# Kernel tuning notes

Measured on AMD Instinct MI355X. Metric: run time of the kernel, lower is better.

Reference implementation:

```python
import jax, jax.numpy as jnp
import numpy as np

N, IN, D, H, C, G = 50000, 128, 64, 4, 10, 64
E_RAND = 800000
NEG_SLOPE = 0.2  # DGL GATConv default LeakyReLU slope


def setup_inputs() -> dict:
    key = jax.random.key(0)
    ks = jax.random.split(key, 20)
    h = jax.random.normal(ks[0], (N, IN), jnp.float32)
    # random edges + self-loops so every dst has at least one in-edge
    src = jnp.concatenate([jax.random.randint(ks[1], (E_RAND,), 0, N), jnp.arange(N)]).astype(jnp.int32)
    dst = jnp.concatenate([jax.random.randint(ks[2], (E_RAND,), 0, N), jnp.arange(N)]).astype(jnp.int32)
    graph_id = jnp.sort(jax.random.randint(ks[3], (N,), 0, G)).astype(jnp.int32)
    w = lambda k, s: jax.random.normal(k, s, jnp.float32) * 0.1
    return {
        "h": h, "src": src, "dst": dst, "graph_id": graph_id,
        "W0": w(ks[4], (IN, H * D)),    "al0": w(ks[5], (H, D)), "ar0": w(ks[6], (H, D)),
        "W1": w(ks[7], (H * D, H * D)), "al1": w(ks[8], (H, D)), "ar1": w(ks[9], (H, D)),
        "W2": w(ks[10], (H * D, H * D)), "al2": w(ks[11], (H, D)), "ar2": w(ks[12], (H, D)),
        "W3": w(ks[13], (H * D, D)),    "al3": w(ks[14], (1, D)), "ar3": w(ks[15], (1, D)),
        "fc1_w": w(ks[16], (D, D)), "fc1_b": jnp.zeros((D,), jnp.float32),
        "fc2_w": w(ks[17], (D, C)), "fc2_b": jnp.zeros((C,), jnp.float32),
    }


def gat_layer(x, W, al, ar, src, dst):
    """DGL GATConv: z=xW; e=LeakyReLU(a_l.z_src + a_r.z_dst); softmax over in-edges of dst; out=sum alpha*z_src."""
    nh, nd = al.shape
    z = (x @ W).reshape(N, nh, nd)                      # [N,H,D]
    el = jnp.sum(z * al, axis=-1)                       # [N,H]
    er = jnp.sum(z * ar, axis=-1)                       # [N,H]
    e = jax.nn.leaky_relu(el[src] + er[dst], NEG_SLOPE)  # [E,H]
    m = jax.ops.segment_max(e, dst, num_segments=N)     # per-dst max (stable softmax)
    ex = jnp.exp(e - m[dst])
    den = jax.ops.segment_sum(ex, dst, num_segments=N)
    alpha = ex / den[dst]                               # [E,H]
    msg = alpha[:, :, None] * z[src]                    # [E,H,D]
    return jax.ops.segment_sum(msg, dst, num_segments=N)  # [N,H,D]


def reference(h, src, dst, graph_id, W0, al0, ar0, W1, al1, ar1, W2, al2, ar2,
              W3, al3, ar3, fc1_w, fc1_b, fc2_w, fc2_b):
    x = jax.nn.relu(gat_layer(h, W0, al0, ar0, src, dst).reshape(N, -1))
    x = jax.nn.relu(gat_layer(x, W1, al1, ar1, src, dst).reshape(N, -1))
    x = jax.nn.relu(gat_layer(x, W2, al2, ar2, src, dst).reshape(N, -1))
    x = jax.nn.relu(gat_layer(x, W3, al3, ar3, src, dst).reshape(N, -1))  # [N,D] (1 head)
    # AvgPooling: mean node features per graph
    counts = jax.ops.segment_sum(jnp.ones((N,), x.dtype), graph_id, num_segments=G)
    pooled = jax.ops.segment_sum(x, graph_id, num_segments=G) / jnp.maximum(counts, 1.0)[:, None]
    y = jax.nn.elu(pooled @ fc1_w + fc1_b)
    y = y @ fc2_w + fc2_b
    return jax.nn.log_softmax(y, axis=0)  # original applies log_softmax over dim=0
```

## Files before the change

### kernel.cpp

```cpp
#include <hip/hip_runtime.h>
#include <hip/hip_bf16.h>
#include <math.h>

#define NN 50000
#define IN_F 128
#define DD 64
#define HH 4
#define CC 10
#define GG 64
#define NEG_SLOPE 0.2f

typedef __attribute__((ext_vector_type(8))) short bf16x8;
typedef __attribute__((ext_vector_type(4))) float f32x4;
typedef __attribute__((ext_vector_type(4))) unsigned short u16x4;

__device__ inline ushort f2bf(float f) {
    unsigned u = __float_as_uint(f);
    unsigned r = (u + 0x7fffu + ((u >> 16) & 1u)) >> 16;
    return (ushort)r;
}
__device__ inline float bf2f(ushort b) { return __uint_as_float(((unsigned)b) << 16); }

__device__ inline float wave_max(float v) {
#pragma unroll
    for (int o = 32; o > 0; o >>= 1) v = fmaxf(v, __shfl_xor(v, o));
    return v;
}
__device__ inline float wave_sum(float v) {
#pragma unroll
    for (int o = 32; o > 0; o >>= 1) v += __shfl_xor(v, o);
    return v;
}

__global__ void hist_kernel(const int* __restrict__ dst, int E, int* __restrict__ counts) {
    int i = blockIdx.x * blockDim.x + threadIdx.x;
    if (i < E) atomicAdd(&counts[dst[i]], 1);
}

__global__ __launch_bounds__(256) void scan_blk(const int* __restrict__ counts,
                                                int* __restrict__ excl,
                                                int* __restrict__ bsum, int n) {
    __shared__ int sh[256];
    int t = threadIdx.x;
    int i = blockIdx.x * 256 + t;
    int v = (i < n) ? counts[i] : 0;
    sh[t] = v;
    __syncthreads();
#pragma unroll
    for (int o = 1; o < 256; o <<= 1) {
        int u = (t >= o) ? sh[t - o] : 0;
        __syncthreads();
        sh[t] += u;
        __syncthreads();
    }
    if (i < n) excl[i] = sh[t] - v;
    if (t == 255) bsum[blockIdx.x] = sh[255];
}

__global__ __launch_bounds__(256) void scan_top(int* __restrict__ bsum, int nb) {
    __shared__ int sh[256];
    int t = threadIdx.x;
    int v = (t < nb) ? bsum[t] : 0;
    sh[t] = v;
    __syncthreads();
#pragma unroll
    for (int o = 1; o < 256; o <<= 1) {
        int u = (t >= o) ? sh[t - o] : 0;
        __syncthreads();
        sh[t] += u;
        __syncthreads();
    }
    if (t < nb) bsum[t] = sh[t] - v;
}

__global__ __launch_bounds__(256) void scan_fin(const int* __restrict__ excl,
                                                const int* __restrict__ bsum,
                                                int* __restrict__ row_ptr,
                                                int* __restrict__ fill, int n, int E) {
    int i = blockIdx.x * blockDim.x + threadIdx.x;
    if (i < n) {
        int r = excl[i] + bsum[i >> 8];
        row_ptr[i] = r;
        fill[i] = r;
    }
    if (i == 0) row_ptr[n] = E;
}

__global__ void scatter_kernel(const int* __restrict__ src, const int* __restrict__ dst,
                               int E, int* __restrict__ fill, int* __restrict__ col_src) {
    int i = blockIdx.x * blockDim.x + threadIdx.x;
    if (i < E) {
        int p = atomicAdd(&fill[dst[i]], 1);
        col_src[p] = src[i];
    }
}

__global__ void wconv_kernel(const float* __restrict__ W, int K, int N,
                             ushort* __restrict__ thi) {
    int i = blockIdx.x * blockDim.x + threadIdx.x;
    if (i >= K * N) return;
    int k = i / N, n = i - k * N;
    size_t o = ((size_t)(k >> 5) * N + n) * 32 + (k & 31);
    thi[o] = f2bf(W[i]);
}

template <int N, int H, bool AF32>
__global__ __launch_bounds__(256) void gemm_mfma_eler(
    const void* __restrict__ A0,
    const ushort* __restrict__ Wthi,
    ushort* __restrict__ zt, const float* __restrict__ al, const float* __restrict__ ar,
    float* __restrict__ el, float* __restrict__ er, int M, int K) {
    constexpr int NT = N / 16;
    __shared__ ushort Bh[2][N][34];
    const int t = threadIdx.x;
    const int w = t >> 6, lane = t & 63;
    const int cl = lane & 15, g = lane >> 4;
    const int bm = blockIdx.x * 64;
    const int arow = bm + 16 * w + cl;
    const bool aval = arow < M;
    const size_t abase = (size_t)arow * K;
    const float* Af = (const float*)A0;
    const ushort* Abf = (const ushort*)A0;

    f32x4 acc[NT];
#pragma unroll
    for (int nt = 0; nt < NT; ++nt) acc[nt] = (f32x4){0.f, 0.f, 0.f, 0.f};

    const int nkb = K >> 5;

    float4 fa0 = {0, 0, 0, 0}, fa1 = {0, 0, 0, 0};
    bf16x8 araw = {0, 0, 0, 0, 0, 0, 0, 0};
    if (aval) {
        if (AF32) {
            fa0 = *(const float4*)(Af + abase + g * 8);
            fa1 = *(const float4*)(Af + abase + g * 8 + 4);
        } else {
            araw = *(const bf16x8*)(Abf + abase + g * 8);
        }
    }
    if (t < N) {
        const float4* gs = (const float4*)(Wthi + (size_t)t * 32);
#pragma unroll
        for (int q = 0; q < 4; ++q) *(float4*)&Bh[0][t][q * 8] = gs[q];
    }
    __syncthreads();

    for (int kb = 0; kb < nkb; ++kb) {
        const int cur = kb & 1;
        bf16x8 a_cur;
        if (AF32) {
            float fv[8] = {fa0.x, fa0.y, fa0.z, fa0.w, fa1.x, fa1.y, fa1.z, fa1.w};
#pragma unroll
            for (int q = 0; q < 8; ++q) a_cur[q] = (short)f2bf(fv[q]);
        } else {
            a_cur = araw;
        }
        float4 rn0, rn1, rn2, rn3;
        const bool pf = (kb + 1 < nkb);
        if (pf && t < N) {
            const float4* gs = (const float4*)(Wthi + ((size_t)(kb + 1) * N + t) * 32);
            rn0 = gs[0]; rn1 = gs[1]; rn2 = gs[2]; rn3 = gs[3];
        }
        if (pf && aval) {
            if (AF32) {
                fa0 = *(const float4*)(Af + abase + (kb + 1) * 32 + g * 8);
                fa1 = *(const float4*)(Af + abase + (kb + 1) * 32 + g * 8 + 4);
            } else {
                araw = *(const bf16x8*)(Abf + abase + (kb + 1) * 32 + g * 8);
            }
        }
#pragma unroll
        for (int nt = 0; nt < NT; ++nt) {
            bf16x8 b_hi = *(const bf16x8*)&Bh[cur][16 * nt + cl][g * 8];
            acc[nt] = __builtin_amdgcn_mfma_f32_16x16x32_bf16(a_cur, b_hi, acc[nt], 0, 0, 0);
        }
        if (pf && t < N) {
            *(float4*)&Bh[cur ^ 1][t][0]  = rn0;
            *(float4*)&Bh[cur ^ 1][t][8]  = rn1;
            *(float4*)&Bh[cur ^ 1][t][16] = rn2;
            *(float4*)&Bh[cur ^ 1][t][24] = rn3;
        }
        __syncthreads();
    }

    const int r0 = bm + 16 * w + 4 * g;
    if (H == 4) {
#pragma unroll
        for (int tt = 0; tt < 4; ++tt) {
#pragma unroll
            for (int j = 0; j < 4; ++j) {
                int r = r0 + j;
                if (r < M) {
                    u16x4 pv;
#pragma unroll
                    for (int h = 0; h < 4; ++h) pv[h] = f2bf(acc[4 * h + tt][j]);
                    *(u16x4*)&zt[(size_t)r * 256 + (16 * tt + cl) * 4] = pv;
                }
            }
        }
    } else {
#pragma unroll
        for (int nt = 0; nt < NT; ++nt) {
#pragma unroll
            for (int j = 0; j < 4; ++j) {
                int r = r0 + j;
                if (r < M) zt[(size_t)r * N + 16 * nt + cl] = f2bf(acc[nt][j]);
            }
        }
    }
#pragma unroll
    for (int h = 0; h < H; ++h) {
        float pl[4] = {0.f, 0.f, 0.f, 0.f};
        float pr[4] = {0.f, 0.f, 0.f, 0.f};
#pragma unroll
        for (int tt = 0; tt < 4; ++tt) {
            int nt = 4 * h + tt;
            float av = al[h * DD + 16 * tt + cl];
            float rv = ar[h * DD + 16 * tt + cl];
#pragma unroll
            for (int j = 0; j < 4; ++j) {
                pl[j] += acc[nt][j] * av;
                pr[j] += acc[nt][j] * rv;
            }
        }
#pragma unroll
        for (int j = 0; j < 4; ++j) {
#pragma unroll
            for (int o = 1; o < 16; o <<= 1) {
                pl[j] += __shfl_xor(pl[j], o);
                pr[j] += __shfl_xor(pr[j], o);
            }
        }
        if (cl == 0) {
#pragma unroll
            for (int j = 0; j < 4; ++j) {
                int r = r0 + j;
                if (r < M) {
                    el[(size_t)r * H + h] = pl[j];
                    er[(size_t)r * H + h] = pr[j];
                }
            }
        }
    }
}

template <int H, bool OUTBF>
__global__ __launch_bounds__(256) void agg_fused(const ushort* __restrict__ zt,
                                                 const float* __restrict__ el,
                                                 const float* __restrict__ er,
                                                 const int* __restrict__ row_ptr,
                                                 const int* __restrict__ col_src,
                                                 float* __restrict__ outf,
                                                 ushort* __restrict__ obf) {
    __shared__ float alf[4][64][H];
    __shared__ int als[4][64];
    const int wid = threadIdx.x >> 6;
    const int lane = threadIdx.x & 63;
    int v = blockIdx.x * 4 + wid;
    if (v >= NN) return;
    int start = row_ptr[v], end = row_ptr[v + 1];
    int deg = end - start;
    float erd[H], acc[H];
#pragma unroll
    for (int h = 0; h < H; ++h) {
        erd[h] = er[(size_t)v * H + h];
        acc[h] = 0.f;
    }

    auto agg_chunk = [&](int cnt) {
        int j = 0;
        for (; j + 4 <= cnt; j += 4) {
            int s0 = als[wid][j + 0], s1 = als[wid][j + 1];
            int s2 = als[wid][j + 2], s3 = als[wid][j + 3];
            if (H == 4) {
                f32x4 a0 = *(const f32x4*)&alf[wid][j + 0][0];
                f32x4 a1 = *(const f32x4*)&alf[wid][j + 1][0];
                f32x4 a2 = *(const f32x4*)&alf[wid][j + 2][0];
                f32x4 a3 = *(const f32x4*)&alf[wid][j + 3][0];
                u16x4 z0 = *(const u16x4*)&zt[(size_t)s0 * 256 + lane * 4];
                u16x4 z1 = *(const u16x4*)&zt[(size_t)s1 * 256 + lane * 4];
                u16x4 z2 = *(const u16x4*)&zt[(size_t)s2 * 256 + lane * 4];
                u16x4 z3 = *(const u16x4*)&zt[(size_t)s3 * 256 + lane * 4];
#pragma unroll
                for (int h = 0; h < 4; ++h) {
                    acc[h] += a0[h] * bf2f(z0[h]);
                    acc[h] += a1[h] * bf2f(z1[h]);
                    acc[h] += a2[h] * bf2f(z2[h]);
                    acc[h] += a3[h] * bf2f(z3[h]);
                }
            } else {
                float a0 = alf[wid][j + 0][0], a1 = alf[wid][j + 1][0];
                float a2 = alf[wid][j + 2][0], a3 = alf[wid][j + 3][0];
                ushort z0 = zt[(size_t)s0 * 64 + lane];
                ushort z1 = zt[(size_t)s1 * 64 + lane];
                ushort z2 = zt[(size_t)s2 * 64 + lane];
                ushort z3 = zt[(size_t)s3 * 64 + lane];
                acc[0] += a0 * bf2f(z0);
                acc[0] += a1 * bf2f(z1);
                acc[0] += a2 * bf2f(z2);
                acc[0] += a3 * bf2f(z3);
            }
        }
        for (; j < cnt; ++j) {
            int s = als[wid][j];
            if (H == 4) {
                f32x4 a = *(const f32x4*)&alf[wid][j][0];
                u16x4 z = *(const u16x4*)&zt[(size_t)s * 256 + lane * 4];
#pragma unroll
                for (int h = 0; h < 4; ++h) acc[h] += a[h] * bf2f(z[h]);
            } else {
                acc[0] += alf[wid][j][0] * bf2f(zt[(size_t)s * 64 + lane]);
            }
        }
    };

    if (deg <= 64) {
        bool valid = lane < deg;
        int s = col_src[valid ? start + lane : start];
        als[wid][lane] = s;
        float e[H];
        if (H == 4) {
            f32x4 ev = *(const f32x4*)&el[(size_t)s * 4];
#pragma unroll
            for (int h = 0; h < 4; ++h) {
                float x = ev[h] + erd[h];
                x = (x >= 0.f) ? x : NEG_SLOPE * x;
                e[h] = valid ? x : -1e30f;
            }
        } else {
            float x = el[s] + erd[0];
            x = (x >= 0.f) ? x : NEG_SLOPE * x;
            e[0] = valid ? x : -1e30f;
        }
#pragma unroll
        for (int h = 0; h < H; ++h) {
            float m = wave_max(e[h]);
            float ex = valid ? __expf(e[h] - m) : 0.f;
            float den = wave_sum(ex);
            alf[wid][lane][h] = ex * (1.f / den);
        }
        __builtin_amdgcn_wave_barrier();
        agg_chunk(deg);
    } else {
        float m[H];
#pragma unroll
        for (int h = 0; h < H; ++h) m[h] = -1e30f;
        for (int base = start; base < end; base += 64) {
            int i = base + lane;
            bool valid = i < end;
            int s = col_src[valid ? i : start];
#pragma unroll
            for (int h = 0; h < H; ++h) {
                float x = el[(size_t)s * H + h] + erd[h];
                x = (x >= 0.f) ? x : NEG_SLOPE * x;
                m[h] = fmaxf(m[h], valid ? x : -1e30f);
            }
        }
        float den[H];
#pragma unroll
        for (int h = 0; h < H; ++h) {
            m[h] = wave_max(m[h]);
            den[h] = 0.f;
        }
        for (int base = start; base < end; base += 64) {
            int i = base + lane;
            bool valid = i < end;
            int s = col_src[valid ? i : start];
#pragma unroll
            for (int h = 0; h < H; ++h) {
                float x = el[(size_t)s * H + h] + erd[h];
                x = (x >= 0.f) ? x : NEG_SLOPE * x;
                den[h] += valid ? __expf(x - m[h]) : 0.f;
            }
        }
        float inv[H];
#pragma unroll
        for (int h = 0; h < H; ++h) inv[h] = 1.f / wave_sum(den[h]);
        for (int base = start; base < end; base += 64) {
            int i = base + lane;
            bool valid = i < end;
            int s = col_src[valid ? i : start];
            als[wid][lane] = s;
#pragma unroll
            for (int h = 0; h < H; ++h) {
                float x = el[(size_t)s * H + h] + erd[h];
                x = (x >= 0.f) ? x : NEG_SLOPE * x;
                alf[wid][lane][h] = valid ? __expf(x - m[h]) * inv[h] : 0.f;
            }
            __builtin_amdgcn_wave_barrier();
            int cnt = min(64, end - base);
            agg_chunk(cnt);
            __builtin_amdgcn_wave_barrier();
        }
    }

#pragma unroll
    for (int h = 0; h < H; ++h) {
        float r = acc[h];
        r = (r > 0.f) ? r : 0.f;
        size_t idx = (size_t)v * H * DD + h * DD + lane;
        if (OUTBF) {
            obf[idx] = f2bf(r);
        } else {
            outf[idx] = r;
        }
    }
}

__device__ inline int lower_bound_dev(const int* a, int n, int v) {
    int lo = 0, hi = n;
    while (lo < hi) {
        int mid = (lo + hi) >> 1;
        if (a[mid] < v) lo = mid + 1; else hi = mid;
    }
    return lo;
}

__global__ __launch_bounds__(256) void pool_kernel(const float* __restrict__ x,
                                                   const int* __restrict__ gid,
                                                   float* __restrict__ pooled,
                                                   float* __restrict__ gcnt) {
    int g = blockIdx.x;
    int start = lower_bound_dev(gid, NN, g);
    int end = lower_bound_dev(gid, NN, g + 1);
    int lane = threadIdx.x & 63;
    int w = threadIdx.x >> 6;
    float acc = 0.f;
    for (int i = start + w; i < end; i += 4) acc += x[(size_t)i * DD + lane];
    __shared__ float red[4][DD];
    red[w][lane] = acc;
    __syncthreads();
    if (w == 0) {
        float s = red[0][lane] + red[1][lane] + red[2][lane] + red[3][lane];
        pooled[g * DD + lane] = s;
        if (lane == 0) gcnt[g] = (float)(end - start);
    }
}

__global__ __launch_bounds__(64) void head_kernel(const float* __restrict__ pooled,
                                                  const float* __restrict__ gcnt,
                                                  const float* __restrict__ fc1w,
                                                  const float* __restrict__ fc1b,
                                                  const float* __restrict__ fc2w,
                                                  const float* __restrict__ fc2b,
                                                  float* __restrict__ out) {
    __shared__ float P[GG][DD + 1];
    __shared__ float Y1[GG][DD + 1];
    int g = threadIdx.x;
    float c = fmaxf(gcnt[g], 1.0f);
    for (int k = 0; k < DD; ++k) P[g][k] = pooled[g * DD + k] / c;
    __syncthreads();
    for (int j = 0; j < DD; ++j) {
        float s = fc1b[j];
        for (int k = 0; k < DD; ++k) s += P[g][k] * fc1w[k * DD + j];
        Y1[g][j] = (s > 0.f) ? s : expm1f(s);
    }
    __syncthreads();
    float y2[CC];
    for (int c2 = 0; c2 < CC; ++c2) {
        float s = fc2b[c2];
        for (int j = 0; j < DD; ++j) s += Y1[g][j] * fc2w[j * CC + c2];
        y2[c2] = s;
    }
    for (int c2 = 0; c2 < CC; ++c2) {
        float m = y2[c2];
#pragma unroll
        for (int o = 32; o > 0; o >>= 1) m = fmaxf(m, __shfl_xor(m, o));
        float sexp = __expf(y2[c2] - m);
#pragma unroll
        for (int o = 32; o > 0; o >>= 1) sexp += __shfl_xor(sexp, o);
        out[g * CC + c2] = y2[c2] - m - logf(sexp);
    }
}

extern "C" void kernel_launch(void* const* d_in, const int* in_sizes, int n_in,
                              void* d_out, int out_size, void* d_ws, size_t ws_size,
                              hipStream_t stream) {
    const float* h    = (const float*)d_in[0];
    const int* src    = (const int*)d_in[1];
    const int* dst    = (const int*)d_in[2];
    const int* gid    = (const int*)d_in[3];
    const float* W0   = (const float*)d_in[4];
    const float* al0  = (const float*)d_in[5];
    const float* ar0  = (const float*)d_in[6];
    const float* W1   = (const float*)d_in[7];
    const float* al1  = (const float*)d_in[8];
    const float* ar1  = (const float*)d_in[9];
    const float* W2   = (const float*)d_in[10];
    const float* al2  = (const float*)d_in[11];
    const float* ar2  = (const float*)d_in[12];
    const float* W3   = (const float*)d_in[13];
    const float* al3  = (const float*)d_in[14];
    const float* ar3  = (const float*)d_in[15];
    const float* fc1w = (const float*)d_in[16];
    const float* fc1b = (const float*)d_in[17];
    const float* fc2w = (const float*)d_in[18];
    const float* fc2b = (const float*)d_in[19];
    const int E = in_sizes[1];

    char* wsb = (char*)d_ws;
    size_t off = 0;
    auto alloc = [&](size_t bytes) -> void* {
        void* p = wsb + off;
        off = (off + bytes + 255) & ~(size_t)255;
        return p;
    };
    ushort* zt      = (ushort*)alloc((size_t)NN * 256 * 2);
    ushort* Abf     = (ushort*)alloc((size_t)NN * 256 * 2);
    float*  bufA    = (float*)alloc((size_t)NN * DD * 4);
    float*  el      = (float*)alloc((size_t)NN * HH * 4);
    float*  er      = (float*)alloc((size_t)NN * HH * 4);
    int*    counts  = (int*)alloc((size_t)NN * 4);
    int*    row_ptr = (int*)alloc((size_t)(NN + 1) * 4);
    int*    fill    = (int*)alloc((size_t)NN * 4);
    int*    excl    = (int*)alloc((size_t)NN * 4);
    int*    bsum    = (int*)alloc((size_t)256 * 4);
    int*    col_src = (int*)alloc((size_t)E * 4);
    float*  pooled  = (float*)alloc((size_t)GG * DD * 4);
    float*  gcnt    = (float*)alloc((size_t)GG * 4);
    ushort* w0h     = (ushort*)alloc((size_t)IN_F * 256 * 2);
    ushort* w1h     = (ushort*)alloc((size_t)256 * 256 * 2);
    ushort* w2h     = (ushort*)alloc((size_t)256 * 256 * 2);
    ushort* w3h     = (ushort*)alloc((size_t)256 * 64 * 2);

    hipMemsetAsync(counts, 0, (size_t)NN * 4, stream);
    int eg = (E + 255) / 256;
    const int nScanBlk = (NN + 255) / 256;
    hist_kernel<<<eg, 256, 0, stream>>>(dst, E, counts);
    scan_blk<<<nScanBlk, 256, 0, stream>>>(counts, excl, bsum, NN);
    scan_top<<<1, 256, 0, stream>>>(bsum, nScanBlk);
    scan_fin<<<nScanBlk, 256, 0, stream>>>(excl, bsum, row_ptr, fill, NN, E);
    scatter_kernel<<<eg, 256, 0, stream>>>(src, dst, E, fill, col_src);

    wconv_kernel<<<(IN_F * 256 + 255) / 256, 256, 0, stream>>>(W0, IN_F, 256, w0h);
    wconv_kernel<<<(256 * 256 + 255) / 256, 256, 0, stream>>>(W1, 256, 256, w1h);
    wconv_kernel<<<(256 * 256 + 255) / 256, 256, 0, stream>>>(W2, 256, 256, w2h);
    wconv_kernel<<<(256 * 64 + 255) / 256, 256, 0, stream>>>(W3, 256, 64, w3h);

    const int gemmGrid = (NN + 63) / 64;
    const int waveBlocks = (NN + 3) / 4;

    gemm_mfma_eler<256, 4, true><<<gemmGrid, 256, 0, stream>>>(h, w0h, zt, al0, ar0, el, er, NN, IN_F);
    agg_fused<4, true><<<waveBlocks, 256, 0, stream>>>(zt, el, er, row_ptr, col_src, nullptr, Abf);

    gemm_mfma_eler<256, 4, false><<<gemmGrid, 256, 0, stream>>>(Abf, w1h, zt, al1, ar1, el, er, NN, 256);
    agg_fused<4, true><<<waveBlocks, 256, 0, stream>>>(zt, el, er, row_ptr, col_src, nullptr, Abf);

    gemm_mfma_eler<256, 4, false><<<gemmGrid, 256, 0, stream>>>(Abf, w2h, zt, al2, ar2, el, er, NN, 256);
    agg_fused<4, true><<<waveBlocks, 256, 0, stream>>>(zt, el, er, row_ptr, col_src, nullptr, Abf);

    gemm_mfma_eler<64, 1, false><<<gemmGrid, 256, 0, stream>>>(Abf, w3h, zt, al3, ar3, el, er, NN, 256);
    agg_fused<1, false><<<waveBlocks, 256, 0, stream>>>(zt, el, er, row_ptr, col_src, bufA, nullptr);

    pool_kernel<<<GG, 256, 0, stream>>>(bufA, gid, pooled, gcnt);
    head_kernel<<<1, 64, 0, stream>>>(pooled, gcnt, fc1w, fc1b, fc2w, fc2b, (float*)d_out);
}
```

Before: 604.5 us.

## Store multi-head projected features as FP8 to halve gather traffic in aggregation

The 4-head layers now write the projected node features z as FP8 (e4m3, packed four per word) instead of bf16, and the aggregation kernel decodes them with the hardware fp8 conversion builtin when it is available. This halves the bytes read by the random per-edge gathers, which dominate aggregation cost, at the price of a large loss in feature precision that may violate tolerance. The change also merges the four weight-conversion launches into a single kernel and widens the pooling kernel from 4 to 16 waves per graph.

```diff
diff --git a/kernel.cpp b/kernel.cpp
--- a/kernel.cpp
+++ b/kernel.cpp
@@ -20,6 +20,39 @@
     return (ushort)r;
 }
 __device__ inline float bf2f(ushort b) { return __uint_as_float(((unsigned)b) << 16); }
+
+__device__ inline unsigned f2fp8(float f) {
+    float a = fabsf(f);
+    a = fminf(a, 448.f);
+    unsigned s = (__float_as_uint(f) >> 31) << 7;
+    unsigned bits;
+    if (a < 0.015625f) {
+        bits = (unsigned)__float2int_rn(a * 512.f);
+    } else {
+        unsigned u = __float_as_uint(a);
+        u += 0x7ffffu + ((u >> 20) & 1u);
+        bits = (u >> 20) - (120u << 3);
+        bits = min(bits, 0x7Eu);
+    }
+    return s | bits;
+}
+
+#if defined(__has_builtin)
+#if __has_builtin(__builtin_amdgcn_cvt_f32_fp8)
+#define HAVE_CVT_FP8 1
+#endif
+#endif
+
+template <int SEL>
+__device__ inline float fp8dec(unsigned w) {
+#ifdef HAVE_CVT_FP8
+    return __builtin_amdgcn_cvt_f32_fp8((int)w, SEL);
+#else
+    unsigned b = (w >> (8 * SEL)) & 0xffu;
+    unsigned u = ((b & 0x80u) << 24) | ((b & 0x7fu) << 20);
+    return __uint_as_float(u) * 0x1p120f;
+#endif
+}
 
 __device__ inline float wave_max(float v) {
 #pragma unroll
@@ -95,20 +128,29 @@
     }
 }
 
-__global__ void wconv_kernel(const float* __restrict__ W, int K, int N,
-                             ushort* __restrict__ thi) {
+__global__ void wconv_all(const float* __restrict__ W0, const float* __restrict__ W1,
+                          const float* __restrict__ W2, const float* __restrict__ W3,
+                          ushort* __restrict__ o0, ushort* __restrict__ o1,
+                          ushort* __restrict__ o2, ushort* __restrict__ o3) {
     int i = blockIdx.x * blockDim.x + threadIdx.x;
-    if (i >= K * N) return;
-    int k = i / N, n = i - k * N;
+    const float* W;
+    ushort* out;
+    int N, rel;
+    if (i < 32768) { W = W0; out = o0; N = 256; rel = i; }
+    else if (i < 98304) { W = W1; out = o1; N = 256; rel = i - 32768; }
+    else if (i < 163840) { W = W2; out = o2; N = 256; rel = i - 98304; }
+    else if (i < 180224) { W = W3; out = o3; N = 64; rel = i - 163840; }
+    else return;
+    int k = rel / N, n = rel - k * N;
     size_t o = ((size_t)(k >> 5) * N + n) * 32 + (k & 31);
-    thi[o] = f2bf(W[i]);
+    out[o] = f2bf(W[rel]);
 }
 
 template <int N, int H, bool AF32>
 __global__ __launch_bounds__(256) void gemm_mfma_eler(
     const void* __restrict__ A0,
     const ushort* __restrict__ Wthi,
-    ushort* __restrict__ zt, const float* __restrict__ al, const float* __restrict__ ar,
+    void* __restrict__ ztv, const float* __restrict__ al, const float* __restrict__ ar,
     float* __restrict__ el, float* __restrict__ er, int M, int K) {
     constexpr int NT = N / 16;
     __shared__ ushort Bh[2][N][34];
@@ -185,20 +227,21 @@
 
     const int r0 = bm + 16 * w + 4 * g;
     if (H == 4) {
+        unsigned char* zf8 = (unsigned char*)ztv;
 #pragma unroll
         for (int tt = 0; tt < 4; ++tt) {
 #pragma unroll
             for (int j = 0; j < 4; ++j) {
                 int r = r0 + j;
                 if (r < M) {
-                    u16x4 pv;
-#pragma unroll
-                    for (int h = 0; h < 4; ++h) pv[h] = f2bf(acc[4 * h + tt][j]);
-                    *(u16x4*)&zt[(size_t)r * 256 + (16 * tt + cl) * 4] = pv;
+                    unsigned pw = f2fp8(acc[tt][j]) | (f2fp8(acc[4 + tt][j]) << 8) |
+                                  (f2fp8(acc[8 + tt][j]) << 16) | (f2fp8(acc[12 + tt][j]) << 24);
+                    *(unsigned*)&zf8[(size_t)r * 256 + (16 * tt + cl) * 4] = pw;
                 }
             }
         }
     } else {
+        ushort* zt = (ushort*)ztv;
 #pragma unroll
         for (int nt = 0; nt < NT; ++nt) {
 #pragma unroll
@@ -245,7 +288,7 @@
 }
 
 template <int H, bool OUTBF>
-__global__ __launch_bounds__(256) void agg_fused(const ushort* __restrict__ zt,
+__global__ __launch_bounds__(256) void agg_fused(const void* __restrict__ ztv,
                                                  const float* __restrict__ el,
                                                  const float* __restrict__ er,
                                                  const int* __restrict__ row_ptr,
@@ -254,6 +297,8 @@
                                                  ushort* __restrict__ obf) {
     __shared__ float alf[4][64][H];
     __shared__ int als[4][64];
+    const unsigned char* zf8 = (const unsigned char*)ztv;
+    const ushort* zt16 = (const ushort*)ztv;
     const int wid = threadIdx.x >> 6;
     const int lane = threadIdx.x & 63;
     int v = blockIdx.x * 4 + wid;
@@ -277,24 +322,21 @@
                 f32x4 a1 = *(const f32x4*)&alf[wid][j + 1][0];
                 f32x4 a2 = *(const f32x4*)&alf[wid][j + 2][0];
                 f32x4 a3 = *(const f32x4*)&alf[wid][j + 3][0];
-                u16x4 z0 = *(const u16x4*)&zt[(size_t)s0 * 256 + lane * 4];
-                u16x4 z1 = *(const u16x4*)&zt[(size_t)s1 * 256 + lane * 4];
-                u16x4 z2 = *(const u16x4*)&zt[(size_t)s2 * 256 + lane * 4];
-                u16x4 z3 = *(const u16x4*)&zt[(size_t)s3 * 256 + lane * 4];
-#pragma unroll
-                for (int h = 0; h < 4; ++h) {
-                    acc[h] += a0[h] * bf2f(z0[h]);
-                    acc[h] += a1[h] * bf2f(z1[h]);
-                    acc[h] += a2[h] * bf2f(z2[h]);
-                    acc[h] += a3[h] * bf2f(z3[h]);
-                }
+                unsigned z0 = *(const unsigned*)&zf8[(size_t)s0 * 256 + lane * 4];
+                unsigned z1 = *(const unsigned*)&zf8[(size_t)s1 * 256 + lane * 4];
+                unsigned z2 = *(const unsigned*)&zf8[(size_t)s2 * 256 + lane * 4];
+                unsigned z3 = *(const unsigned*)&zf8[(size_t)s3 * 256 + lane * 4];
+                acc[0] += a0[0] * fp8dec<0>(z0) + a1[0] * fp8dec<0>(z1) + a2[0] * fp8dec<0>(z2) + a3[0] * fp8dec<0>(z3);
+                acc[1] += a0[1] * fp8dec<1>(z0) + a1[1] * fp8dec<1>(z1) + a2[1] * fp8dec<1>(z2) + a3[1] * fp8dec<1>(z3);
+                acc[2] += a0[2] * fp8dec<2>(z0) + a1[2] * fp8dec<2>(z1) + a2[2] * fp8dec<2>(z2) + a3[2] * fp8dec<2>(z3);
+                acc[3] += a0[3] * fp8dec<3>(z0) + a1[3] * fp8dec<3>(z1) + a2[3] * fp8dec<3>(z2) + a3[3] * fp8dec<3>(z3);
             } else {
                 float a0 = alf[wid][j + 0][0], a1 = alf[wid][j + 1][0];
                 float a2 = alf[wid][j + 2][0], a3 = alf[wid][j + 3][0];
-                ushort z0 = zt[(size_t)s0 * 64 + lane];
-                ushort z1 = zt[(size_t)s1 * 64 + lane];
-                ushort z2 = zt[(size_t)s2 * 64 + lane];
-                ushort z3 = zt[(size_t)s3 * 64 + lane];
+                ushort z0 = zt16[(size_t)s0 * 64 + lane];
+                ushort z1 = zt16[(size_t)s1 * 64 + lane];
+                ushort z2 = zt16[(size_t)s2 * 64 + lane];
+                ushort z3 = zt16[(size_t)s3 * 64 + lane];
                 acc[0] += a0 * bf2f(z0);
                 acc[0] += a1 * bf2f(z1);
                 acc[0] += a2 * bf2f(z2);
@@ -305,11 +347,13 @@
             int s = als[wid][j];
             if (H == 4) {
                 f32x4 a = *(const f32x4*)&alf[wid][j][0];
-                u16x4 z = *(const u16x4*)&zt[(size_t)s * 256 + lane * 4];
-#pragma unroll
-                for (int h = 0; h < 4; ++h) acc[h] += a[h] * bf2f(z[h]);
+                unsigned z = *(const unsigned*)&zf8[(size_t)s * 256 + lane * 4];
+                acc[0] += a[0] * fp8dec<0>(z);
+                acc[1] += a[1] * fp8dec<1>(z);
+                acc[2] += a[2] * fp8dec<2>(z);
+                acc[3] += a[3] * fp8dec<3>(z);
             } else {
-                acc[0] += alf[wid][j][0] * bf2f(zt[(size_t)s * 64 + lane]);
+                acc[0] += alf[wid][j][0] * bf2f(zt16[(size_t)s * 64 + lane]);
             }
         }
     };
@@ -416,22 +460,24 @@
     return lo;
 }
 
-__global__ __launch_bounds__(256) void pool_kernel(const float* __restrict__ x,
-                                                   const int* __restrict__ gid,
-                                                   float* __restrict__ pooled,
-                                                   float* __restrict__ gcnt) {
+__global__ __launch_bounds__(1024) void pool_kernel(const float* __restrict__ x,
+                                                    const int* __restrict__ gid,
+                                                    float* __restrict__ pooled,
+                                                    float* __restrict__ gcnt) {
     int g = blockIdx.x;
     int start = lower_bound_dev(gid, NN, g);
     int end = lower_bound_dev(gid, NN, g + 1);
     int lane = threadIdx.x & 63;
     int w = threadIdx.x >> 6;
     float acc = 0.f;
-    for (int i = start + w; i < end; i += 4) acc += x[(size_t)i * DD + lane];
-    __shared__ float red[4][DD];
+    for (int i = start + w; i < end; i += 16) acc += x[(size_t)i * DD + lane];
+    __shared__ float red[16][DD];
     red[w][lane] = acc;
     __syncthreads();
     if (w == 0) {
-        float s = red[0][lane] + red[1][lane] + red[2][lane] + red[3][lane];
+        float s = 0.f;
+#pragma unroll
+        for (int q = 0; q < 16; ++q) s += red[q][lane];
         pooled[g * DD + lane] = s;
         if (lane == 0) gcnt[g] = (float)(end - start);
     }
@@ -505,7 +551,8 @@
         off = (off + bytes + 255) & ~(size_t)255;
         return p;
     };
-    ushort* zt      = (ushort*)alloc((size_t)NN * 256 * 2);
+    unsigned char* zf8 = (unsigned char*)alloc((size_t)NN * 256);
+    ushort* zt16    = (ushort*)alloc((size_t)NN * DD * 2);
     ushort* Abf     = (ushort*)alloc((size_t)NN * 256 * 2);
     float*  bufA    = (float*)alloc((size_t)NN * DD * 4);
     float*  el      = (float*)alloc((size_t)NN * HH * 4);
@@ -532,26 +579,23 @@
     scan_fin<<<nScanBlk, 256, 0, stream>>>(excl, bsum, row_ptr, fill, NN, E);
     scatter_kernel<<<eg, 256, 0, stream>>>(src, dst, E, fill, col_src);
 
-    wconv_kernel<<<(IN_F * 256 + 255) / 256, 256, 0, stream>>>(W0, IN_F, 256, w0h);
-    wconv_kernel<<<(256 * 256 + 255) / 256, 256, 0, stream>>>(W1, 256, 256, w1h);
-    wconv_kernel<<<(256 * 256 + 255) / 256, 256, 0, stream>>>(W2, 256, 256, w2h);
-    wconv_kernel<<<(256 * 64 + 255) / 256, 256, 0, stream>>>(W3, 256, 64, w3h);
+    wconv_all<<<(180224 + 255) / 256, 256, 0, stream>>>(W0, W1, W2, W3, w0h, w1h, w2h, w3h);
 
     const int gemmGrid = (NN + 63) / 64;
     const int waveBlocks = (NN + 3) / 4;
 
-    gemm_mfma_eler<256, 4, true><<<gemmGrid, 256, 0, stream>>>(h, w0h, zt, al0, ar0, el, er, NN, IN_F);
-    agg_fused<4, true><<<waveBlocks, 256, 0, stream>>>(zt, el, er, row_ptr, col_src, nullptr, Abf);
-
-    gemm_mfma_eler<256, 4, false><<<gemmGrid, 256, 0, stream>>>(Abf, w1h, zt, al1, ar1, el, er, NN, 256);
-    agg_fused<4, true><<<waveBlocks, 256, 0, stream>>>(zt, el, er, row_ptr, col_src, nullptr, Abf);
-
-    gemm_mfma_eler<256, 4, false><<<gemmGrid, 256, 0, stream>>>(Abf, w2h, zt, al2, ar2, el, er, NN, 256);
-    agg_fused<4, true><<<waveBlocks, 256, 0, stream>>>(zt, el, er, row_ptr, col_src, nullptr, Abf);
-
-    gemm_mfma_eler<64, 1, false><<<gemmGrid, 256, 0, stream>>>(Abf, w3h, zt, al3, ar3, el, er, NN, 256);
-    agg_fused<1, false><<<waveBlocks, 256, 0, stream>>>(zt, el, er, row_ptr, col_src, bufA, nullptr);
-
-    pool_kernel<<<GG, 256, 0, stream>>>(bufA, gid, pooled, gcnt);
+    gemm_mfma_eler<256, 4, true><<<gemmGrid, 256, 0, stream>>>(h, w0h, zf8, al0, ar0, el, er, NN, IN_F);
+    agg_fused<4, true><<<waveBlocks, 256, 0, stream>>>(zf8, el, er, row_ptr, col_src, nullptr, Abf);
+
+    gemm_mfma_eler<256, 4, false><<<gemmGrid, 256, 0, stream>>>(Abf, w1h, zf8, al1, ar1, el, er, NN, 256);
+    agg_fused<4, true><<<waveBlocks, 256, 0, stream>>>(zf8, el, er, row_ptr, col_src, nullptr, Abf);
+
+    gemm_mfma_eler<256, 4, false><<<gemmGrid, 256, 0, stream>>>(Abf, w2h, zf8, al2, ar2, el, er, NN, 256);
+    agg_fused<4, true><<<waveBlocks, 256, 0, stream>>>(zf8, el, er, row_ptr, col_src, nullptr, Abf);
+
+    gemm_mfma_eler<64, 1, false><<<gemmGrid, 256, 0, stream>>>(Abf, w3h, zt16, al3, ar3, el, er, NN, 256);
+    agg_fused<1, false><<<waveBlocks, 256, 0, stream>>>(zt16, el, er, row_ptr, col_src, bufA, nullptr);
+
+    pool_kernel<<<GG, 1024, 0, stream>>>(bufA, gid, pooled, gcnt);
     head_kernel<<<1, 64, 0, stream>>>(pooled, gcnt, fc1w, fc1b, fc2w, fc2b, (float*)d_out);
 }
```

Result: faster. 531.7 us (-12.0%).
